# Kernel tuning notes

Measured on AMD Instinct MI355X. Metric: run time of the kernel, lower is better.

Reference implementation:

```python
import jax, jax.numpy as jnp
import numpy as np

N = 10                      # number of spline knots (init arg n)
STEP = 1.0 / (N - 1.0)      # knot spacing
NVALS = 255                 # torch.arange(0, 1, 1/255) -> 255 samples


def _spline_matrix(n):
    # Faithful port of NeuralSplineBase._precalc (natural cubic spline system)
    step = 1.0 / (n - 1.0)
    mat = 4.0 * np.eye(n - 2)
    np.fill_diagonal(mat[1:, :-1], 1.0)
    np.fill_diagonal(mat[:-1, 1:], 1.0)
    A = 6.0 * np.linalg.inv(mat) / step ** 2
    z = np.zeros(n - 2)
    A = np.vstack([z, A, z])                 # [n, n-2]
    B = np.zeros([n - 2, n])
    np.fill_diagonal(B, 1.0)
    np.fill_diagonal(B[:, 1:], -2.0)
    np.fill_diagonal(B[:, 2:], 1.0)
    return (A @ B).astype(np.float32)        # [n, n]

MAT = jnp.asarray(_spline_matrix(N))


def _coeffs(ys_total):
    # ys_total: [..., N] -> cubic poly coeffs a,b,c,d each [..., N-1]
    h = STEP
    M = jnp.einsum('ij,...j->...i', MAT, ys_total)          # second derivatives
    a = (M[..., 1:] - M[..., :-1]) / (6.0 * h)
    b = M[..., :-1] / 2.0
    c = (ys_total[..., 1:] - ys_total[..., :-1]) / h - (M[..., 1:] + 2.0 * M[..., :-1]) * (h / 6.0)
    d = ys_total[..., :-1]
    return a, b, c, d


def _eval(a, b, c, d, x):
    # a..d: [B,E,C,N-1]; x: [B,1,C,P] or [1,1,1,P] -> y: [B,E,C,P]
    B, E, C = a.shape[:3]
    P = x.shape[-1]
    xi = jnp.floor(jnp.clip(x / STEP, 0.0, N - 2)).astype(jnp.int32)
    xf = x - xi.astype(x.dtype) * STEP
    xib = jnp.broadcast_to(xi, (B, E, C, P))
    ag = jnp.take_along_axis(a, xib, axis=-1)
    bg = jnp.take_along_axis(b, xib, axis=-1)
    cg = jnp.take_along_axis(c, xib, axis=-1)
    dg = jnp.take_along_axis(d, xib, axis=-1)
    return ((ag * xf + bg) * xf + cg) * xf + dg


def setup_inputs() -> dict:
    key = jax.random.key(0)
    k1, k2 = jax.random.split(key)
    batch = jax.random.uniform(k1, (8, 3, 768, 768), dtype=jnp.float32)
    ys = jax.random.normal(k2, (8, 3, 3, N), dtype=jnp.float32) * 0.05  # residual knot offsets
    return {"batch": batch, "ys": ys}


def reference(batch, ys):
    B, C, H, W = batch.shape
    E = ys.shape[1]
    identity = jnp.arange(N, dtype=batch.dtype) / (N - 1.0)
    a, b, c, d = _coeffs(ys + identity)                 # [B,E,C,N-1]
    # enhance images
    x = batch.reshape(B, 1, C, H * W)
    out = _eval(a, b, c, d, x).reshape(B, E, C, H, W)
    # spline curves sampled on [0, 1)
    vals = (jnp.arange(NVALS, dtype=batch.dtype) / 255.0).reshape(1, 1, 1, NVALS)
    splines = _eval(a, b, c, d, vals)                   # [B,E,C,255]
    return out, splines
```

## Files before the change

### kernel.cpp

```cpp
#include <hip/hip_runtime.h>

#define B_DIM 8
#define E_DIM 3
#define C_DIM 3
#define N_KNOTS 10
#define NSEG 9
#define NVALS 255
#define HW 589824
#define HW4 147456
#define OUT1_ELEMS 42467328
constexpr float STEPF = 1.0f / 9.0f;

__global__ __launch_bounds__(256) void spline_coeffs_kernel(
    const float* __restrict__ ys, float4* __restrict__ ws,
    float* __restrict__ splines_out)
{
    const int s = blockIdx.x;
    __shared__ float4 coef[NSEG];

    if (threadIdx.x == 0) {
        float y[N_KNOTS];
#pragma unroll
        for (int j = 0; j < N_KNOTS; ++j)
            y[j] = ys[s * N_KNOTS + j] + (float)j * STEPF;

        float r[8];
#pragma unroll
        for (int i = 0; i < 8; ++i)
            r[i] = 486.0f * (y[i] - 2.0f * y[i + 1] + y[i + 2]);

        float cp[8], dp[8];
        cp[0] = 0.25f;
        dp[0] = r[0] * 0.25f;
#pragma unroll
        for (int i = 1; i < 8; ++i) {
            float m = 1.0f / (4.0f - cp[i - 1]);
            cp[i] = m;
            dp[i] = (r[i] - dp[i - 1]) * m;
        }
        float M[N_KNOTS];
        M[0] = 0.0f;
        M[9] = 0.0f;
        M[8] = dp[7];
#pragma unroll
        for (int i = 6; i >= 0; --i)
            M[i + 1] = dp[i] - cp[i] * M[i + 2];

#pragma unroll
        for (int k = 0; k < NSEG; ++k) {
            float4 cf;
            cf.x = (M[k + 1] - M[k]) * 1.5f;
            cf.y = M[k] * 0.5f;
            cf.z = (y[k + 1] - y[k]) * 9.0f
                   - (M[k + 1] + 2.0f * M[k]) * (1.0f / 54.0f);
            cf.w = y[k];
            coef[k] = cf;
            ws[s * NSEG + k] = cf;
        }
    }
    __syncthreads();

    const int t = threadIdx.x;
    if (t < NVALS) {
        float v = (float)t * (1.0f / 255.0f);
        float tx = fminf(fmaxf(v * 9.0f, 0.0f), 8.0f);
        float xif = floorf(tx);
        int xi = (int)xif;
        float xf = v - xif * STEPF;
        float4 cf = coef[xi];
        splines_out[s * NVALS + t] =
            ((cf.x * xf + cf.y) * xf + cf.z) * xf + cf.w;
    }
}

__device__ __forceinline__ void eval3(float x, const float4 (&coef)[3][NSEG],
                                      float& o0, float& o1, float& o2)
{
    float tx = fminf(fmaxf(x * 9.0f, 0.0f), 8.0f);
    float xif = floorf(tx);
    int xi = (int)xif;
    float xf = x - xif * STEPF;
    float4 c0 = coef[0][xi];
    float4 c1 = coef[1][xi];
    float4 c2 = coef[2][xi];
    o0 = ((c0.x * xf + c0.y) * xf + c0.z) * xf + c0.w;
    o1 = ((c1.x * xf + c1.y) * xf + c1.z) * xf + c1.w;
    o2 = ((c2.x * xf + c2.y) * xf + c2.z) * xf + c2.w;
}

__global__ __launch_bounds__(256) void spline_eval_kernel(
    const float4* __restrict__ batch, const float4* __restrict__ ws,
    float4* __restrict__ out)
{
    const int plane = blockIdx.y;
    const int b = plane / 3;
    const int c = plane % 3;

    __shared__ float4 coef[E_DIM][NSEG];
    const int t = threadIdx.x;
    if (t < E_DIM * NSEG) {
        int e = t / NSEG, k = t % NSEG;
        coef[e][k] = ws[(b * 9 + e * 3 + c) * NSEG + k];
    }
    __syncthreads();

    const float4* src = batch + (size_t)plane * HW4;
    float4* dst0 = out + (size_t)(b * 9 + 0 * 3 + c) * HW4;
    float4* dst1 = out + (size_t)(b * 9 + 1 * 3 + c) * HW4;
    float4* dst2 = out + (size_t)(b * 9 + 2 * 3 + c) * HW4;

    const int idx0 = blockIdx.x * 1024 + t;
#pragma unroll
    for (int kk = 0; kk < 4; ++kk) {
        int idx = idx0 + kk * 256;
        float4 x = src[idx];
        float4 r0, r1, r2;
        eval3(x.x, coef, r0.x, r1.x, r2.x);
        eval3(x.y, coef, r0.y, r1.y, r2.y);
        eval3(x.z, coef, r0.z, r1.z, r2.z);
        eval3(x.w, coef, r0.w, r1.w, r2.w);
        dst0[idx] = r0;
        dst1[idx] = r1;
        dst2[idx] = r2;
    }
}

extern "C" void kernel_launch(void* const* d_in, const int* in_sizes, int n_in,
                              void* d_out, int out_size, void* d_ws, size_t ws_size,
                              hipStream_t stream)
{
    const float* batch = (const float*)d_in[0];
    const float* ys = (const float*)d_in[1];
    float* out = (float*)d_out;
    float4* ws = (float4*)d_ws;

    spline_coeffs_kernel<<<dim3(B_DIM * E_DIM * C_DIM), dim3(256), 0, stream>>>(
        ys, ws, out + OUT1_ELEMS);

    spline_eval_kernel<<<dim3(144, 24), dim3(256), 0, stream>>>(
        (const float4*)batch, (const float4*)ws, (float4*)out);
}
```

Before: 43.48 us.

## Fuse spline coefficient solve into eval kernel and use nontemporal stores

Removes the separate coefficient kernel: every eval block now solves the tridiagonal system for its three E-channels in shared memory. Block x=0 of each plane also writes the sampled spline curves. Output stores become nontemporal, aiming to reduce cache pollution for the large streaming write. This saves one kernel launch and the workspace round trip, at the cost of redundant serial coefficient work in every block before the barrier.

```diff
diff --git a/kernel.cpp b/kernel.cpp
--- a/kernel.cpp
+++ b/kernel.cpp
@@ -1,28 +1,31 @@
 #include <hip/hip_runtime.h>
 
-#define B_DIM 8
-#define E_DIM 3
-#define C_DIM 3
-#define N_KNOTS 10
 #define NSEG 9
 #define NVALS 255
-#define HW 589824
 #define HW4 147456
 #define OUT1_ELEMS 42467328
 constexpr float STEPF = 1.0f / 9.0f;
 
-__global__ __launch_bounds__(256) void spline_coeffs_kernel(
-    const float* __restrict__ ys, float4* __restrict__ ws,
-    float* __restrict__ splines_out)
+typedef float f32x4 __attribute__((ext_vector_type(4)));
+
+__global__ __launch_bounds__(256) void spline_fused_kernel(
+    const float4* __restrict__ batch, const float* __restrict__ ys,
+    float* __restrict__ out)
 {
-    const int s = blockIdx.x;
-    __shared__ float4 coef[NSEG];
+    const int plane = blockIdx.y;
+    const int b = plane / 3;
+    const int c = plane - b * 3;
 
-    if (threadIdx.x == 0) {
-        float y[N_KNOTS];
+    __shared__ float4 coef[3][NSEG];
+    const int t = threadIdx.x;
+
+    if (t < 3) {
+        const int e = t;
+        const float* yp = ys + ((size_t)(b * 3 + e) * 3 + c) * 10;
+        float y[10];
 #pragma unroll
-        for (int j = 0; j < N_KNOTS; ++j)
-            y[j] = ys[s * N_KNOTS + j] + (float)j * STEPF;
+        for (int j = 0; j < 10; ++j)
+            y[j] = yp[j] + (float)j * STEPF;
 
         float r[8];
 #pragma unroll
@@ -38,10 +41,8 @@
             cp[i] = m;
             dp[i] = (r[i] - dp[i - 1]) * m;
         }
-        float M[N_KNOTS];
-        M[0] = 0.0f;
-        M[9] = 0.0f;
-        M[8] = dp[7];
+        float M[10];
+        M[0] = 0.0f; M[9] = 0.0f; M[8] = dp[7];
 #pragma unroll
         for (int i = 6; i >= 0; --i)
             M[i + 1] = dp[i] - cp[i] * M[i + 2];
@@ -54,74 +55,52 @@
             cf.z = (y[k + 1] - y[k]) * 9.0f
                    - (M[k + 1] + 2.0f * M[k]) * (1.0f / 54.0f);
             cf.w = y[k];
-            coef[k] = cf;
-            ws[s * NSEG + k] = cf;
+            coef[e][k] = cf;
         }
     }
     __syncthreads();
 
-    const int t = threadIdx.x;
-    if (t < NVALS) {
+    if (blockIdx.x == 0 && t < NVALS) {
         float v = (float)t * (1.0f / 255.0f);
-        float tx = fminf(fmaxf(v * 9.0f, 0.0f), 8.0f);
-        float xif = floorf(tx);
+        float xif = floorf(fminf(v * 9.0f, 8.0f));
         int xi = (int)xif;
         float xf = v - xif * STEPF;
-        float4 cf = coef[xi];
-        splines_out[s * NVALS + t] =
-            ((cf.x * xf + cf.y) * xf + cf.z) * xf + cf.w;
+        float* sp = out + OUT1_ELEMS;
+#pragma unroll
+        for (int e = 0; e < 3; ++e) {
+            float4 cf = coef[e][xi];
+            sp[((size_t)(b * 3 + e) * 3 + c) * NVALS + t] =
+                ((cf.x * xf + cf.y) * xf + cf.z) * xf + cf.w;
+        }
     }
-}
-
-__device__ __forceinline__ void eval3(float x, const float4 (&coef)[3][NSEG],
-                                      float& o0, float& o1, float& o2)
-{
-    float tx = fminf(fmaxf(x * 9.0f, 0.0f), 8.0f);
-    float xif = floorf(tx);
-    int xi = (int)xif;
-    float xf = x - xif * STEPF;
-    float4 c0 = coef[0][xi];
-    float4 c1 = coef[1][xi];
-    float4 c2 = coef[2][xi];
-    o0 = ((c0.x * xf + c0.y) * xf + c0.z) * xf + c0.w;
-    o1 = ((c1.x * xf + c1.y) * xf + c1.z) * xf + c1.w;
-    o2 = ((c2.x * xf + c2.y) * xf + c2.z) * xf + c2.w;
-}
-
-__global__ __launch_bounds__(256) void spline_eval_kernel(
-    const float4* __restrict__ batch, const float4* __restrict__ ws,
-    float4* __restrict__ out)
-{
-    const int plane = blockIdx.y;
-    const int b = plane / 3;
-    const int c = plane % 3;
-
-    __shared__ float4 coef[E_DIM][NSEG];
-    const int t = threadIdx.x;
-    if (t < E_DIM * NSEG) {
-        int e = t / NSEG, k = t % NSEG;
-        coef[e][k] = ws[(b * 9 + e * 3 + c) * NSEG + k];
-    }
-    __syncthreads();
 
     const float4* src = batch + (size_t)plane * HW4;
-    float4* dst0 = out + (size_t)(b * 9 + 0 * 3 + c) * HW4;
-    float4* dst1 = out + (size_t)(b * 9 + 1 * 3 + c) * HW4;
-    float4* dst2 = out + (size_t)(b * 9 + 2 * 3 + c) * HW4;
+    f32x4* dst0 = (f32x4*)out + (size_t)(b * 9 + 0 + c) * HW4;
+    f32x4* dst1 = (f32x4*)out + (size_t)(b * 9 + 3 + c) * HW4;
+    f32x4* dst2 = (f32x4*)out + (size_t)(b * 9 + 6 + c) * HW4;
 
     const int idx0 = blockIdx.x * 1024 + t;
 #pragma unroll
     for (int kk = 0; kk < 4; ++kk) {
         int idx = idx0 + kk * 256;
         float4 x = src[idx];
-        float4 r0, r1, r2;
-        eval3(x.x, coef, r0.x, r1.x, r2.x);
-        eval3(x.y, coef, r0.y, r1.y, r2.y);
-        eval3(x.z, coef, r0.z, r1.z, r2.z);
-        eval3(x.w, coef, r0.w, r1.w, r2.w);
-        dst0[idx] = r0;
-        dst1[idx] = r1;
-        dst2[idx] = r2;
+        f32x4 r0, r1, r2;
+#pragma unroll
+        for (int l = 0; l < 4; ++l) {
+            float xv = (&x.x)[l];
+            float xif = floorf(fminf(fmaxf(xv * 9.0f, 0.0f), 8.0f));
+            int xi = (int)xif;
+            float xf = xv - xif * STEPF;
+            float4 c0 = coef[0][xi];
+            float4 c1 = coef[1][xi];
+            float4 c2 = coef[2][xi];
+            r0[l] = ((c0.x * xf + c0.y) * xf + c0.z) * xf + c0.w;
+            r1[l] = ((c1.x * xf + c1.y) * xf + c1.z) * xf + c1.w;
+            r2[l] = ((c2.x * xf + c2.y) * xf + c2.z) * xf + c2.w;
+        }
+        __builtin_nontemporal_store(r0, dst0 + idx);
+        __builtin_nontemporal_store(r1, dst1 + idx);
+        __builtin_nontemporal_store(r2, dst2 + idx);
     }
 }
 
@@ -132,11 +111,7 @@
     const float* batch = (const float*)d_in[0];
     const float* ys = (const float*)d_in[1];
     float* out = (float*)d_out;
-    float4* ws = (float4*)d_ws;
 
-    spline_coeffs_kernel<<<dim3(B_DIM * E_DIM * C_DIM), dim3(256), 0, stream>>>(
-        ys, ws, out + OUT1_ELEMS);
-
-    spline_eval_kernel<<<dim3(144, 24), dim3(256), 0, stream>>>(
-        (const float4*)batch, (const float4*)ws, (float4*)out);
+    spline_fused_kernel<<<dim3(144, 24), dim3(256), 0, stream>>>(
+        (const float4*)batch, ys, out);
 }
```

Measured after the change: 39.50 us. 9.1% less time.
